# Optimization experiments

Hardware: AMD Instinct MI355X
Metric: run time of the kernel (lower is better)

## Reference

```python
import jax, jax.numpy as jnp
import numpy as np

NUM_NODES = 1_200_000
NUM_FILLER = 200_000
NUM_PHYS = NUM_NODES - NUM_FILLER  # 1,000,000 physical nodes
NUM_MOVABLE = 900_000
NBX = NBY = 512
XL, XH, YL, YH = 0.0, 1000.0, 0.0, 1000.0
BSX = (XH - XL) / NBX
BSY = (YH - YL) / NBY
PIN_STRETCH = 1.4142135623730951
UNIT_PIN_CAP = 0.05
MAX_RATE = 1.5
MIN_RATE = 1.0 / MAX_RATE
K = 5  # max bins overlapped per dimension (span<=4.0, bin~1.95)


def _overlap_terms(lo, hi, bin_size, origin, nb):
    # lo, hi: [n] interval per node. Returns bin indices [n,K] and overlap lengths [n,K].
    il = jnp.clip(jnp.floor((lo - origin) / bin_size).astype(jnp.int32), 0, nb - 1)
    idx = il[:, None] + jnp.arange(K, dtype=jnp.int32)[None, :]
    valid = idx < nb
    idx = jnp.clip(idx, 0, nb - 1)
    b_lo = origin + idx.astype(lo.dtype) * bin_size
    ov = jnp.maximum(jnp.minimum(hi[:, None], b_lo + bin_size) - jnp.maximum(lo[:, None], b_lo), 0.0)
    return idx, jnp.where(valid, ov, 0.0)


def _forward(pos, node_size_x, node_size_y, flat_node2pin_start_map):
    P = NUM_PHYS
    sx, sy = node_size_x[:P], node_size_y[:P]
    # stretched half sizes: at least half a stretched bin
    hx = 0.5 * jnp.maximum(BSX * PIN_STRETCH, sx)
    hy = 0.5 * jnp.maximum(BSY * PIN_STRETCH, sy)
    cx = pos[:P] + 0.5 * sx
    cy = pos[NUM_NODES:NUM_NODES + P] + 0.5 * sy
    pw = (flat_node2pin_start_map[1:P + 1] - flat_node2pin_start_map[:P]).astype(pos.dtype)
    density = pw / (4.0 * hx * hy)  # pins per unit area over stretched bbox

    # stage 1: scatter stretched-bbox pin density into bin map
    ix, ovx = _overlap_terms(cx - hx, cx + hx, BSX, XL, NBX)  # [P,K]
    iy, ovy = _overlap_terms(cy - hy, cy + hy, BSY, YL, NBY)  # [P,K]
    contrib = ovx[:, :, None] * ovy[:, None, :] * density[:, None, None]  # [P,K,K]
    flat_idx = (ix[:, :, None] * NBY + iy[:, None, :]).reshape(-1)
    pin_map = jnp.zeros(NBX * NBY, dtype=pos.dtype).at[flat_idx].add(contrib.reshape(-1))

    # stage 2: pin utilization per bin, clamped adjust rate
    util = jnp.clip(pin_map / (BSX * BSY * UNIT_PIN_CAP), MIN_RATE, MAX_RATE)

    # stage 3: per movable node, integrate utilization over its (unstretched) bbox
    M = NUM_MOVABLE
    x_lo = pos[:M]
    x_hi = x_lo + node_size_x[:M]
    y_lo = pos[NUM_NODES:NUM_NODES + M]
    y_hi = y_lo + node_size_y[:M]
    jx, wx = _overlap_terms(x_lo, x_hi, BSX, XL, NBX)  # [M,K]
    jy, wy = _overlap_terms(y_lo, y_hi, BSY, YL, NBY)  # [M,K]
    u = util[jx[:, :, None] * NBY + jy[:, None, :]]  # [M,K,K]
    instance_pin_area = jnp.sum(wx[:, :, None] * wy[:, None, :] * u, axis=(1, 2))
    return instance_pin_area


def setup_inputs() -> dict:
    key = jax.random.key(0)
    k1, k2, k3, k4 = jax.random.split(key, 4)
    node_size_x = jax.random.uniform(k1, (NUM_NODES,), jnp.float32, 1.0, 4.0)
    node_size_y = jnp.full((NUM_NODES,), 2.0, jnp.float32)  # row height
    px = jax.random.uniform(k2, (NUM_NODES,), jnp.float32, 0.0, 995.0)
    py = jax.random.uniform(k3, (NUM_NODES,), jnp.float32, 0.0, 995.0)
    pos = jnp.concatenate([px, py])
    pin_counts = jax.random.randint(k4, (NUM_PHYS,), 1, 9, jnp.int32)
    flat = jnp.concatenate([jnp.zeros(1, jnp.int32), jnp.cumsum(pin_counts).astype(jnp.int32)])
    return {"pos": pos, "node_size_x": node_size_x, "node_size_y": node_size_y,
            "flat_node2pin_start_map": flat}


def reference(pos, node_size_x, node_size_y, flat_node2pin_start_map):
    return _forward(pos, node_size_x, node_size_y, flat_node2pin_start_map)
```

## Files before the change

kernel.cpp:

```cpp
#include <hip/hip_runtime.h>

#define NUM_NODES   1200000
#define NUM_FILLER  200000
#define NUM_PHYS    (NUM_NODES - NUM_FILLER)
#define NUM_MOVABLE 900000
#define NBX 512
#define NBY 512
#define NBINS (NBX * NBY)
#define BSX 1.953125f
#define BSY 1.953125f
#define PIN_STRETCH 1.4142135623730951f
#define CAP 0.19073486328125f
#define INV_CAP (1.0f / 0.19073486328125f)
#define MAX_RATE 1.5f
#define MIN_RATE (1.0f/1.5f)
#define K 5

#define TBITS   5
#define TSZ     32
#define TDIM    16
#define NTILES  (TDIM * TDIM)
#define HALO    3
#define LTS     (TSZ + HALO)
#define NPB     2048
#define NBLK    ((NUM_PHYS + NPB - 1) / NPB)
#define CAPSLOT 6144

__device__ __forceinline__ int bin_lo(float lo) {
    int il = (int)floorf(lo / BSX);
    return min(max(il, 0), NBX - 1);
}

__global__ __launch_bounds__(256) void sort_pass(
    const float* __restrict__ pos,
    const float* __restrict__ nsx,
    const float* __restrict__ nsy,
    const int*   __restrict__ flat,
    int*         __restrict__ tileCursor,
    float4*      __restrict__ sorted4,
    float*       __restrict__ dens)
{
    __shared__ int cnt[NTILES];
    __shared__ int basep[NTILES];
    int tid = threadIdx.x;
    cnt[tid] = 0;
    __syncthreads();

    float lox[NPB/256], loy[NPB/256], hix[NPB/256], hiy[NPB/256], dn[NPB/256];
    int tl[NPB/256];
    int base = blockIdx.x * NPB;
    #pragma unroll
    for (int it = 0; it < NPB / 256; ++it) {
        int i = base + it * 256 + tid;
        tl[it] = -1;
        if (i < NUM_PHYS) {
            float sx = nsx[i], sy = nsy[i];
            float hx = 0.5f * fmaxf(BSX * PIN_STRETCH, sx);
            float hy = 0.5f * fmaxf(BSY * PIN_STRETCH, sy);
            float cx = pos[i] + 0.5f * sx;
            float cy = pos[NUM_NODES + i] + 0.5f * sy;
            float pw = (float)(flat[i + 1] - flat[i]);
            dn[it]  = pw / (4.0f * hx * hy);
            lox[it] = cx - hx; hix[it] = cx + hx;
            loy[it] = cy - hy; hiy[it] = cy + hy;
            int il = bin_lo(lox[it]), jl = bin_lo(loy[it]);
            tl[it] = ((il >> TBITS) << 4) | (jl >> TBITS);
            atomicAdd(&cnt[tl[it]], 1);
        }
    }
    __syncthreads();
    int c = cnt[tid];
    int b = (c > 0) ? atomicAdd(&tileCursor[tid], c) : 0;
    basep[tid] = b;
    __syncthreads();
    #pragma unroll
    for (int it = 0; it < NPB / 256; ++it) {
        if (tl[it] >= 0) {
            int slot = atomicAdd(&basep[tl[it]], 1);
            if (slot < CAPSLOT) {
                size_t g = (size_t)tl[it] * CAPSLOT + slot;
                sorted4[g] = make_float4(lox[it], loy[it], hix[it], hiy[it]);
                dens[g] = dn[it];
            }
        }
    }
}

__global__ __launch_bounds__(1024) void accumulate_tiles(
    const float4* __restrict__ sorted4,
    const float*  __restrict__ dens,
    const int*    __restrict__ tileCursor,
    float*        __restrict__ pin)
{
    __shared__ float tileA[LTS * LTS];
    int tid = threadIdx.x;
    int t = blockIdx.x;
    int bx0 = (t >> 4) * TSZ, by0 = (t & 15) * TSZ;

    for (int i = tid; i < LTS * LTS; i += 1024) tileA[i] = 0.0f;
    __syncthreads();

    int cnt = min(tileCursor[t], CAPSLOT);
    size_t b0 = (size_t)t * CAPSLOT;
    for (int i = tid; i < cnt; i += 1024) {
        float4 r = sorted4[b0 + i];
        float d = dens[b0 + i];
        int il = bin_lo(r.x), jl = bin_lo(r.y);
        int ie = min(min((int)floorf(r.z / BSX), NBX - 1), il + HALO);
        int je = min(min((int)floorf(r.w / BSY), NBY - 1), jl + HALO);
        int lr = il - bx0, lc = jl - by0;
        for (int a = il; a <= ie; ++a) {
            float blo = (float)a * BSX;
            float ox = fmaxf(fminf(r.z, blo + BSX) - fmaxf(r.x, blo), 0.0f);
            int rowb = (lr + (a - il)) * LTS + lc;
            for (int b2 = jl; b2 <= je; ++b2) {
                float blo2 = (float)b2 * BSY;
                float oy = fmaxf(fminf(r.w, blo2 + BSY) - fmaxf(r.y, blo2), 0.0f);
                float cc = ox * oy * d;
                if (cc != 0.0f) atomicAdd(&tileA[rowb + (b2 - jl)], cc);
            }
        }
    }
    __syncthreads();
    for (int i = tid; i < LTS * LTS; i += 1024) {
        float v = tileA[i];
        if (v != 0.0f) {
            int r = i / LTS, c = i % LTS;
            int gx = bx0 + r, gy = by0 + c;
            if (gx < NBX && gy < NBY) atomicAdd(&pin[gx * NBY + gy], v);
        }
    }
}

__global__ __launch_bounds__(256) void gather_pin_area(
    const float* __restrict__ pos,
    const float* __restrict__ nsx,
    const float* __restrict__ nsy,
    const float* __restrict__ pin,
    float*       __restrict__ out)
{
    int m = blockIdx.x * blockDim.x + threadIdx.x;
    if (m >= NUM_MOVABLE) return;

    float xlo = pos[m];
    float xhi = xlo + nsx[m];
    float ylo = pos[NUM_NODES + m];
    float yhi = ylo + nsy[m];

    int il = bin_lo(xlo);
    int ie = min(min((int)floorf(xhi / BSX), NBX - 1), il + K - 1);
    int jl = bin_lo(ylo);
    int je = min(min((int)floorf(yhi / BSY), NBY - 1), jl + K - 1);

    float acc = 0.0f;
    for (int a = il; a <= ie; ++a) {
        float blo = (float)a * BSX;
        float wxv = fmaxf(fminf(xhi, blo + BSX) - fmaxf(xlo, blo), 0.0f);
        const float* __restrict__ row = pin + a * NBY;
        for (int b2 = jl; b2 <= je; ++b2) {
            float blo2 = (float)b2 * BSY;
            float wyv = fmaxf(fminf(yhi, blo2 + BSY) - fmaxf(ylo, blo2), 0.0f);
            float u = fminf(fmaxf(row[b2] * INV_CAP, MIN_RATE), MAX_RATE);
            acc += wxv * wyv * u;
        }
    }
    out[m] = acc;
}

__global__ __launch_bounds__(256) void scatter_pin_map_agent(
    const float* __restrict__ pos,
    const float* __restrict__ nsx,
    const float* __restrict__ nsy,
    const int*   __restrict__ flat,
    float*       __restrict__ map)
{
    int p = blockIdx.x * blockDim.x + threadIdx.x;
    if (p >= NUM_PHYS) return;
    float sx = nsx[p], sy = nsy[p];
    float hx = 0.5f * fmaxf(BSX * PIN_STRETCH, sx);
    float hy = 0.5f * fmaxf(BSY * PIN_STRETCH, sy);
    float cx = pos[p] + 0.5f * sx;
    float cy = pos[NUM_NODES + p] + 0.5f * sy;
    float pw = (float)(flat[p + 1] - flat[p]);
    float density = pw / (4.0f * hx * hy);
    float lox = cx - hx, hixv = cx + hx;
    float loy = cy - hy, hiyv = cy + hy;
    int il = bin_lo(lox), jl = bin_lo(loy);
    int ie = min(min((int)floorf(hixv / BSX), NBX - 1), il + K - 1);
    int je = min(min((int)floorf(hiyv / BSY), NBY - 1), jl + K - 1);
    for (int a = il; a <= ie; ++a) {
        float blo = (float)a * BSX;
        float ox = fmaxf(fminf(hixv, blo + BSX) - fmaxf(lox, blo), 0.0f);
        for (int b = jl; b <= je; ++b) {
            float blo2 = (float)b * BSY;
            float oy = fmaxf(fminf(hiyv, blo2 + BSY) - fmaxf(loy, blo2), 0.0f);
            float c = ox * oy * density;
            if (c != 0.0f) atomicAdd(&map[a * NBY + b], c);
        }
    }
}

extern "C" void kernel_launch(void* const* d_in, const int* in_sizes, int n_in,
                              void* d_out, int out_size, void* d_ws, size_t ws_size,
                              hipStream_t stream) {
    const float* pos  = (const float*)d_in[0];
    const float* nsx  = (const float*)d_in[1];
    const float* nsy  = (const float*)d_in[2];
    const int*   flat = (const int*)d_in[3];
    float* out = (float*)d_out;

    float* pin = (float*)d_ws;
    int* tileCursor = (int*)((char*)d_ws + (size_t)NBINS * 4);
    float4* sorted4 = (float4*)((char*)d_ws + (size_t)NBINS * 4 + 8192);
    float* dens = (float*)(sorted4 + (size_t)NTILES * CAPSLOT);
    size_t needed = (size_t)NBINS * 4 + 8192
                  + (size_t)NTILES * CAPSLOT * 20;

    dim3 blk(256);
    if (ws_size >= needed) {
        hipMemsetAsync(d_ws, 0, (size_t)NBINS * 4 + 8192, stream);
        sort_pass<<<NBLK, blk, 0, stream>>>(pos, nsx, nsy, flat, tileCursor, sorted4, dens);
        accumulate_tiles<<<NTILES, dim3(1024), 0, stream>>>(sorted4, dens, tileCursor, pin);
    } else {
        hipMemsetAsync(pin, 0, (size_t)NBINS * 4, stream);
        scatter_pin_map_agent<<<(NUM_PHYS + 255) / 256, blk, 0, stream>>>(pos, nsx, nsy, flat, pin);
    }
    gather_pin_area<<<(NUM_MOVABLE + 255) / 256, blk, 0, stream>>>(pos, nsx, nsy, pin, out);
}
```

Measured before the change: 149.5 us.

## Bin-sort movable nodes by tile and gather utilization from shared-memory patches

The sort pass now also buckets movable nodes into 32x32-bin tiles, writing their bboxes and original indices alongside the physical-node records. A new tiled gather kernel loads each tile's clamped utilization patch (with halo) into LDS once, then integrates over it for every node in the tile and scatters each result back to its original index. The aim is to replace random global reads of the pin map with LDS reads. In exchange it adds a second sorted buffer to write and read, scattered output writes, only 256 gather blocks, and per-tile capacity limits that drop nodes if a tile overflows. The halo also grows from 3 to 4.

Result: slower. 156.0 us (+4.3%).

```diff
diff --git a/kernel.cpp b/kernel.cpp
--- a/kernel.cpp
+++ b/kernel.cpp
@@ -20,76 +20,103 @@
 #define TSZ     32
 #define TDIM    16
 #define NTILES  (TDIM * TDIM)
-#define HALO    3
+#define HALO    (K - 1)
 #define LTS     (TSZ + HALO)
 #define NPB     2048
 #define NBLK    ((NUM_PHYS + NPB - 1) / NPB)
-#define CAPSLOT 6144
+#define CAPP    6144
+#define CAPM    5120
 
 __device__ __forceinline__ int bin_lo(float lo) {
     int il = (int)floorf(lo / BSX);
     return min(max(il, 0), NBX - 1);
 }
 
-__global__ __launch_bounds__(256) void sort_pass(
+__global__ __launch_bounds__(256) void sort_both(
     const float* __restrict__ pos,
     const float* __restrict__ nsx,
     const float* __restrict__ nsy,
     const int*   __restrict__ flat,
-    int*         __restrict__ tileCursor,
-    float4*      __restrict__ sorted4,
-    float*       __restrict__ dens)
-{
-    __shared__ int cnt[NTILES];
-    __shared__ int basep[NTILES];
+    int*         __restrict__ physCur,
+    int*         __restrict__ movCur,
+    float4*      __restrict__ physRec,
+    float*       __restrict__ physDens,
+    float4*      __restrict__ movRec,
+    int*         __restrict__ movIdx)
+{
+    __shared__ int cntP[NTILES], cntM[NTILES], baseP[NTILES], baseM[NTILES];
     int tid = threadIdx.x;
-    cnt[tid] = 0;
-    __syncthreads();
-
-    float lox[NPB/256], loy[NPB/256], hix[NPB/256], hiy[NPB/256], dn[NPB/256];
-    int tl[NPB/256];
+    cntP[tid] = 0; cntM[tid] = 0;
+    __syncthreads();
+
+    float px[NPB/256], py[NPB/256], sx[NPB/256], sy[NPB/256], dn[NPB/256];
+    int pk[NPB/256];
     int base = blockIdx.x * NPB;
     #pragma unroll
     for (int it = 0; it < NPB / 256; ++it) {
         int i = base + it * 256 + tid;
-        tl[it] = -1;
+        int k = 0;
         if (i < NUM_PHYS) {
-            float sx = nsx[i], sy = nsy[i];
-            float hx = 0.5f * fmaxf(BSX * PIN_STRETCH, sx);
-            float hy = 0.5f * fmaxf(BSY * PIN_STRETCH, sy);
-            float cx = pos[i] + 0.5f * sx;
-            float cy = pos[NUM_NODES + i] + 0.5f * sy;
+            float pxv = pos[i], pyv = pos[NUM_NODES + i];
+            float sxv = nsx[i], syv = nsy[i];
+            float hx = 0.5f * fmaxf(BSX * PIN_STRETCH, sxv);
+            float hy = 0.5f * fmaxf(BSY * PIN_STRETCH, syv);
             float pw = (float)(flat[i + 1] - flat[i]);
-            dn[it]  = pw / (4.0f * hx * hy);
-            lox[it] = cx - hx; hix[it] = cx + hx;
-            loy[it] = cy - hy; hiy[it] = cy + hy;
-            int il = bin_lo(lox[it]), jl = bin_lo(loy[it]);
-            tl[it] = ((il >> TBITS) << 4) | (jl >> TBITS);
-            atomicAdd(&cnt[tl[it]], 1);
-        }
-    }
-    __syncthreads();
-    int c = cnt[tid];
-    int b = (c > 0) ? atomicAdd(&tileCursor[tid], c) : 0;
-    basep[tid] = b;
-    __syncthreads();
+            px[it] = pxv; py[it] = pyv; sx[it] = sxv; sy[it] = syv;
+            dn[it] = pw / (4.0f * hx * hy);
+            float lox = pxv + 0.5f * sxv - hx;
+            float loy = pyv + 0.5f * syv - hy;
+            int tp = ((bin_lo(lox) >> TBITS) << 4) | (bin_lo(loy) >> TBITS);
+            atomicAdd(&cntP[tp], 1);
+            k = 0x10000 | tp;
+            if (i < NUM_MOVABLE) {
+                int tm = ((bin_lo(pxv) >> TBITS) << 4) | (bin_lo(pyv) >> TBITS);
+                atomicAdd(&cntM[tm], 1);
+                k |= 0x20000 | (tm << 8);
+            }
+        }
+        pk[it] = k;
+    }
+    __syncthreads();
+    int cp = cntP[tid], cm = cntM[tid];
+    baseP[tid] = (cp > 0) ? atomicAdd(&physCur[tid], cp) : 0;
+    baseM[tid] = (cm > 0) ? atomicAdd(&movCur[tid],  cm) : 0;
+    __syncthreads();
+    int i0 = base + tid;
     #pragma unroll
     for (int it = 0; it < NPB / 256; ++it) {
-        if (tl[it] >= 0) {
-            int slot = atomicAdd(&basep[tl[it]], 1);
-            if (slot < CAPSLOT) {
-                size_t g = (size_t)tl[it] * CAPSLOT + slot;
-                sorted4[g] = make_float4(lox[it], loy[it], hix[it], hiy[it]);
-                dens[g] = dn[it];
+        int k = pk[it];
+        if (k & 0x10000) {
+            float sxv = sx[it], syv = sy[it];
+            float hx = 0.5f * fmaxf(BSX * PIN_STRETCH, sxv);
+            float hy = 0.5f * fmaxf(BSY * PIN_STRETCH, syv);
+            float lox = px[it] + 0.5f * sxv - hx;
+            float loy = py[it] + 0.5f * syv - hy;
+            int tp = k & 0xFF;
+            int s = atomicAdd(&baseP[tp], 1);
+            if (s < CAPP) {
+                size_t g = (size_t)tp * CAPP + s;
+                physRec[g] = make_float4(lox, loy, lox + 2.0f * hx, loy + 2.0f * hy);
+                physDens[g] = dn[it];
+            }
+        }
+        if (k & 0x20000) {
+            int tm = (k >> 8) & 0xFF;
+            int s = atomicAdd(&baseM[tm], 1);
+            if (s < CAPM) {
+                size_t g = (size_t)tm * CAPM + s;
+                movRec[g] = make_float4(px[it], py[it],
+                                        px[it] + sx[it], py[it] + sy[it]);
+                movIdx[g] = i0 + it * 256;
             }
         }
     }
 }
 
 __global__ __launch_bounds__(1024) void accumulate_tiles(
-    const float4* __restrict__ sorted4,
-    const float*  __restrict__ dens,
-    const int*    __restrict__ tileCursor,
+    const float4* __restrict__ physRec,
+    const float*  __restrict__ physDens,
+    const int*    __restrict__ physCur,
     float*        __restrict__ pin)
 {
     __shared__ float tileA[LTS * LTS];
@@ -100,11 +127,11 @@
     for (int i = tid; i < LTS * LTS; i += 1024) tileA[i] = 0.0f;
     __syncthreads();
 
-    int cnt = min(tileCursor[t], CAPSLOT);
-    size_t b0 = (size_t)t * CAPSLOT;
+    int cnt = min(physCur[t], CAPP);
+    size_t b0 = (size_t)t * CAPP;
     for (int i = tid; i < cnt; i += 1024) {
-        float4 r = sorted4[b0 + i];
-        float d = dens[b0 + i];
+        float4 r = physRec[b0 + i];
+        float d = physDens[b0 + i];
         int il = bin_lo(r.x), jl = bin_lo(r.y);
         int ie = min(min((int)floorf(r.z / BSX), NBX - 1), il + HALO);
         int je = min(min((int)floorf(r.w / BSY), NBY - 1), jl + HALO);
@@ -132,39 +159,50 @@
     }
 }
 
-__global__ __launch_bounds__(256) void gather_pin_area(
-    const float* __restrict__ pos,
-    const float* __restrict__ nsx,
-    const float* __restrict__ nsy,
-    const float* __restrict__ pin,
-    float*       __restrict__ out)
-{
-    int m = blockIdx.x * blockDim.x + threadIdx.x;
-    if (m >= NUM_MOVABLE) return;
-
-    float xlo = pos[m];
-    float xhi = xlo + nsx[m];
-    float ylo = pos[NUM_NODES + m];
-    float yhi = ylo + nsy[m];
-
-    int il = bin_lo(xlo);
-    int ie = min(min((int)floorf(xhi / BSX), NBX - 1), il + K - 1);
-    int jl = bin_lo(ylo);
-    int je = min(min((int)floorf(yhi / BSY), NBY - 1), jl + K - 1);
-
-    float acc = 0.0f;
-    for (int a = il; a <= ie; ++a) {
-        float blo = (float)a * BSX;
-        float wxv = fmaxf(fminf(xhi, blo + BSX) - fmaxf(xlo, blo), 0.0f);
-        const float* __restrict__ row = pin + a * NBY;
-        for (int b2 = jl; b2 <= je; ++b2) {
-            float blo2 = (float)b2 * BSY;
-            float wyv = fmaxf(fminf(yhi, blo2 + BSY) - fmaxf(ylo, blo2), 0.0f);
-            float u = fminf(fmaxf(row[b2] * INV_CAP, MIN_RATE), MAX_RATE);
-            acc += wxv * wyv * u;
-        }
-    }
-    out[m] = acc;
+__global__ __launch_bounds__(1024) void gather_tiled(
+    const float4* __restrict__ movRec,
+    const int*    __restrict__ movIdx,
+    const int*    __restrict__ movCur,
+    const float*  __restrict__ pin,
+    float*        __restrict__ out)
+{
+    __shared__ float patch[LTS * LTS];
+    int tid = threadIdx.x;
+    int t = blockIdx.x;
+    int bx0 = (t >> 4) * TSZ, by0 = (t & 15) * TSZ;
+
+    for (int i = tid; i < LTS * LTS; i += 1024) {
+        int r = i / LTS, c = i % LTS;
+        int gx = bx0 + r, gy = by0 + c;
+        float u = MIN_RATE;
+        if (gx < NBX && gy < NBY)
+            u = fminf(fmaxf(pin[gx * NBY + gy] * INV_CAP, MIN_RATE), MAX_RATE);
+        patch[i] = u;
+    }
+    __syncthreads();
+
+    int cnt = min(movCur[t], CAPM);
+    size_t b0 = (size_t)t * CAPM;
+    for (int i = tid; i < cnt; i += 1024) {
+        float4 r = movRec[b0 + i];
+        int idx = movIdx[b0 + i];
+        int il = bin_lo(r.x), jl = bin_lo(r.y);
+        int ie = min(min((int)floorf(r.z / BSX), NBX - 1), il + K - 1);
+        int je = min(min((int)floorf(r.w / BSY), NBY - 1), jl + K - 1);
+        int lr = il - bx0, lc = jl - by0;
+        float acc = 0.0f;
+        for (int a = il; a <= ie; ++a) {
+            float blo = (float)a * BSX;
+            float wxv = fmaxf(fminf(r.z, blo + BSX) - fmaxf(r.x, blo), 0.0f);
+            int rowb = (lr + (a - il)) * LTS + lc;
+            for (int b2 = jl; b2 <= je; ++b2) {
+                float blo2 = (float)b2 * BSY;
+                float wyv = fmaxf(fminf(r.w, blo2 + BSY) - fmaxf(r.y, blo2), 0.0f);
+                acc += wxv * wyv * patch[rowb + (b2 - jl)];
+            }
+        }
+        out[idx] = acc;
+    }
 }
 
 __global__ __launch_bounds__(256) void scatter_pin_map_agent(
@@ -200,6 +238,38 @@
     }
 }
 
+__global__ __launch_bounds__(256) void gather_direct(
+    const float* __restrict__ pos,
+    const float* __restrict__ nsx,
+    const float* __restrict__ nsy,
+    const float* __restrict__ pin,
+    float*       __restrict__ out)
+{
+    int m = blockIdx.x * blockDim.x + threadIdx.x;
+    if (m >= NUM_MOVABLE) return;
+    float xlo = pos[m];
+    float xhi = xlo + nsx[m];
+    float ylo = pos[NUM_NODES + m];
+    float yhi = ylo + nsy[m];
+    int il = bin_lo(xlo);
+    int ie = min(min((int)floorf(xhi / BSX), NBX - 1), il + K - 1);
+    int jl = bin_lo(ylo);
+    int je = min(min((int)floorf(yhi / BSY), NBY - 1), jl + K - 1);
+    float acc = 0.0f;
+    for (int a = il; a <= ie; ++a) {
+        float blo = (float)a * BSX;
+        float wxv = fmaxf(fminf(xhi, blo + BSX) - fmaxf(xlo, blo), 0.0f);
+        const float* __restrict__ row = pin + a * NBY;
+        for (int b2 = jl; b2 <= je; ++b2) {
+            float blo2 = (float)b2 * BSY;
+            float wyv = fmaxf(fminf(yhi, blo2 + BSY) - fmaxf(ylo, blo2), 0.0f);
+            float u = fminf(fmaxf(row[b2] * INV_CAP, MIN_RATE), MAX_RATE);
+            acc += wxv * wyv * u;
+        }
+    }
+    out[m] = acc;
+}
+
 extern "C" void kernel_launch(void* const* d_in, const int* in_sizes, int n_in,
                               void* d_out, int out_size, void* d_ws, size_t ws_size,
                               hipStream_t stream) {
@@ -209,21 +279,28 @@
     const int*   flat = (const int*)d_in[3];
     float* out = (float*)d_out;
 
-    float* pin = (float*)d_ws;
-    int* tileCursor = (int*)((char*)d_ws + (size_t)NBINS * 4);
-    float4* sorted4 = (float4*)((char*)d_ws + (size_t)NBINS * 4 + 8192);
-    float* dens = (float*)(sorted4 + (size_t)NTILES * CAPSLOT);
+    char* wsb = (char*)d_ws;
+    float*  pin      = (float*)wsb;
+    int*    physCur  = (int*)(wsb + (size_t)NBINS * 4);
+    int*    movCur   = physCur + NTILES;
+    float4* physRec  = (float4*)(wsb + (size_t)NBINS * 4 + 8192);
+    float*  physDens = (float*)(physRec + (size_t)NTILES * CAPP);
+    float4* movRec   = (float4*)(physDens + (size_t)NTILES * CAPP);
+    int*    movIdx   = (int*)(movRec + (size_t)NTILES * CAPM);
     size_t needed = (size_t)NBINS * 4 + 8192
-                  + (size_t)NTILES * CAPSLOT * 20;
+                  + (size_t)NTILES * CAPP * 20 + (size_t)NTILES * CAPM * 20;
 
     dim3 blk(256);
     if (ws_size >= needed) {
         hipMemsetAsync(d_ws, 0, (size_t)NBINS * 4 + 8192, stream);
-        sort_pass<<<NBLK, blk, 0, stream>>>(pos, nsx, nsy, flat, tileCursor, sorted4, dens);
-        accumulate_tiles<<<NTILES, dim3(1024), 0, stream>>>(sorted4, dens, tileCursor, pin);
+        sort_both<<<NBLK, blk, 0, stream>>>(pos, nsx, nsy, flat,
+                                            physCur, movCur,
+                                            physRec, physDens, movRec, movIdx);
+        accumulate_tiles<<<NTILES, dim3(1024), 0, stream>>>(physRec, physDens, physCur, pin);
+        gather_tiled<<<NTILES, dim3(1024), 0, stream>>>(movRec, movIdx, movCur, pin, out);
     } else {
         hipMemsetAsync(pin, 0, (size_t)NBINS * 4, stream);
         scatter_pin_map_agent<<<(NUM_PHYS + 255) / 256, blk, 0, stream>>>(pos, nsx, nsy, flat, pin);
-    }
-    gather_pin_area<<<(NUM_MOVABLE + 255) / 256, blk, 0, stream>>>(pos, nsx, nsy, pin, out);
-}
+        gather_direct<<<(NUM_MOVABLE + 255) / 256, blk, 0, stream>>>(pos, nsx, nsy, pin, out);
+    }
+}
```

## Partition tile cursors per XCD, enlarge sort blocks, store interior bins directly

Applied to the files above, without the earlier changes.

The bucketing pass now reads the hardware XCC ID and gives each tile a separate cursor and record region per XCD. This is meant to cut cross-die contention on the global atomic cursors. The sort kernel also switches to 1024-thread blocks, each handling 4096 nodes, so fewer blocks issue global cursor atomics. In the accumulate kernel, each tile walks all eight XCD sub-buckets, writes interior bins with plain stores, and keeps atomics only for halo bins. The cost is a larger workspace, a per-tile loop over eight regions, and reliance on an inline-asm hardware register read.

Result: no change. 146.9 us (-1.8%).

```diff
diff --git a/kernel.cpp b/kernel.cpp
--- a/kernel.cpp
+++ b/kernel.cpp
@@ -20,66 +20,75 @@
 #define TSZ     32
 #define TDIM    16
 #define NTILES  (TDIM * TDIM)
-#define HALO    3
+#define HALO    (K - 1)
 #define LTS     (TSZ + HALO)
-#define NPB     2048
+#define NXCD    8
+#define SBLK    1024
+#define NPB     4096
+#define IPT     (NPB / SBLK)
 #define NBLK    ((NUM_PHYS + NPB - 1) / NPB)
-#define CAPSLOT 6144
+#define CAPX    1024
 
 __device__ __forceinline__ int bin_lo(float lo) {
     int il = (int)floorf(lo / BSX);
     return min(max(il, 0), NBX - 1);
 }
 
-__global__ __launch_bounds__(256) void sort_pass(
+__global__ __launch_bounds__(SBLK) void sort_phys(
     const float* __restrict__ pos,
     const float* __restrict__ nsx,
     const float* __restrict__ nsy,
     const int*   __restrict__ flat,
-    int*         __restrict__ tileCursor,
-    float4*      __restrict__ sorted4,
+    int*         __restrict__ cur,
+    float4*      __restrict__ rec,
     float*       __restrict__ dens)
 {
     __shared__ int cnt[NTILES];
     __shared__ int basep[NTILES];
     int tid = threadIdx.x;
-    cnt[tid] = 0;
-    __syncthreads();
-
-    float lox[NPB/256], loy[NPB/256], hix[NPB/256], hiy[NPB/256], dn[NPB/256];
-    int tl[NPB/256];
+    if (tid < NTILES) cnt[tid] = 0;
+    __syncthreads();
+
+    unsigned xcc;
+    asm volatile("s_getreg_b32 %0, hwreg(HW_REG_XCC_ID, 0, 32)" : "=s"(xcc));
+    xcc &= (NXCD - 1);
+
+    float lox[IPT], loy[IPT], hix[IPT], hiy[IPT], dn[IPT];
+    int tl[IPT];
     int base = blockIdx.x * NPB;
     #pragma unroll
-    for (int it = 0; it < NPB / 256; ++it) {
-        int i = base + it * 256 + tid;
+    for (int it = 0; it < IPT; ++it) {
+        int i = base + it * SBLK + tid;
         tl[it] = -1;
         if (i < NUM_PHYS) {
-            float sx = nsx[i], sy = nsy[i];
-            float hx = 0.5f * fmaxf(BSX * PIN_STRETCH, sx);
-            float hy = 0.5f * fmaxf(BSY * PIN_STRETCH, sy);
-            float cx = pos[i] + 0.5f * sx;
-            float cy = pos[NUM_NODES + i] + 0.5f * sy;
+            float sxv = nsx[i], syv = nsy[i];
+            float hx = 0.5f * fmaxf(BSX * PIN_STRETCH, sxv);
+            float hy = 0.5f * fmaxf(BSY * PIN_STRETCH, syv);
+            float cx = pos[i] + 0.5f * sxv;
+            float cy = pos[NUM_NODES + i] + 0.5f * syv;
             float pw = (float)(flat[i + 1] - flat[i]);
             dn[it]  = pw / (4.0f * hx * hy);
             lox[it] = cx - hx; hix[it] = cx + hx;
             loy[it] = cy - hy; hiy[it] = cy + hy;
-            int il = bin_lo(lox[it]), jl = bin_lo(loy[it]);
-            tl[it] = ((il >> TBITS) << 4) | (jl >> TBITS);
-            atomicAdd(&cnt[tl[it]], 1);
-        }
-    }
-    __syncthreads();
-    int c = cnt[tid];
-    int b = (c > 0) ? atomicAdd(&tileCursor[tid], c) : 0;
-    basep[tid] = b;
+            int t = ((bin_lo(lox[it]) >> TBITS) << 4) | (bin_lo(loy[it]) >> TBITS);
+            tl[it] = t;
+            atomicAdd(&cnt[t], 1);
+        }
+    }
+    __syncthreads();
+    if (tid < NTILES) {
+        int c = cnt[tid];
+        basep[tid] = (c > 0) ? atomicAdd(&cur[tid * NXCD + xcc], c) : 0;
+    }
     __syncthreads();
     #pragma unroll
-    for (int it = 0; it < NPB / 256; ++it) {
-        if (tl[it] >= 0) {
-            int slot = atomicAdd(&basep[tl[it]], 1);
-            if (slot < CAPSLOT) {
-                size_t g = (size_t)tl[it] * CAPSLOT + slot;
-                sorted4[g] = make_float4(lox[it], loy[it], hix[it], hiy[it]);
+    for (int it = 0; it < IPT; ++it) {
+        int t = tl[it];
+        if (t >= 0) {
+            int s = atomicAdd(&basep[t], 1);
+            if (s < CAPX) {
+                size_t g = ((size_t)t * NXCD + xcc) * CAPX + s;
+                rec[g] = make_float4(lox[it], loy[it], hix[it], hiy[it]);
                 dens[g] = dn[it];
             }
         }
@@ -87,9 +96,9 @@
 }
 
 __global__ __launch_bounds__(1024) void accumulate_tiles(
-    const float4* __restrict__ sorted4,
+    const float4* __restrict__ rec,
     const float*  __restrict__ dens,
-    const int*    __restrict__ tileCursor,
+    const int*    __restrict__ cur,
     float*        __restrict__ pin)
 {
     __shared__ float tileA[LTS * LTS];
@@ -100,34 +109,40 @@
     for (int i = tid; i < LTS * LTS; i += 1024) tileA[i] = 0.0f;
     __syncthreads();
 
-    int cnt = min(tileCursor[t], CAPSLOT);
-    size_t b0 = (size_t)t * CAPSLOT;
-    for (int i = tid; i < cnt; i += 1024) {
-        float4 r = sorted4[b0 + i];
-        float d = dens[b0 + i];
-        int il = bin_lo(r.x), jl = bin_lo(r.y);
-        int ie = min(min((int)floorf(r.z / BSX), NBX - 1), il + HALO);
-        int je = min(min((int)floorf(r.w / BSY), NBY - 1), jl + HALO);
-        int lr = il - bx0, lc = jl - by0;
-        for (int a = il; a <= ie; ++a) {
-            float blo = (float)a * BSX;
-            float ox = fmaxf(fminf(r.z, blo + BSX) - fmaxf(r.x, blo), 0.0f);
-            int rowb = (lr + (a - il)) * LTS + lc;
-            for (int b2 = jl; b2 <= je; ++b2) {
-                float blo2 = (float)b2 * BSY;
-                float oy = fmaxf(fminf(r.w, blo2 + BSY) - fmaxf(r.y, blo2), 0.0f);
-                float cc = ox * oy * d;
-                if (cc != 0.0f) atomicAdd(&tileA[rowb + (b2 - jl)], cc);
+    for (int x = 0; x < NXCD; ++x) {
+        int cnt = min(cur[t * NXCD + x], CAPX);
+        size_t b0 = ((size_t)t * NXCD + x) * CAPX;
+        for (int i = tid; i < cnt; i += 1024) {
+            float4 r = rec[b0 + i];
+            float d = dens[b0 + i];
+            int il = bin_lo(r.x), jl = bin_lo(r.y);
+            int ie = min(min((int)floorf(r.z / BSX), NBX - 1), il + HALO);
+            int je = min(min((int)floorf(r.w / BSY), NBY - 1), jl + HALO);
+            int lr = il - bx0, lc = jl - by0;
+            for (int a = il; a <= ie; ++a) {
+                float blo = (float)a * BSX;
+                float ox = fmaxf(fminf(r.z, blo + BSX) - fmaxf(r.x, blo), 0.0f);
+                int rowb = (lr + (a - il)) * LTS + lc;
+                for (int b2 = jl; b2 <= je; ++b2) {
+                    float blo2 = (float)b2 * BSY;
+                    float oy = fmaxf(fminf(r.w, blo2 + BSY) - fmaxf(r.y, blo2), 0.0f);
+                    float cc = ox * oy * d;
+                    if (cc != 0.0f) atomicAdd(&tileA[rowb + (b2 - jl)], cc);
+                }
             }
         }
     }
     __syncthreads();
     for (int i = tid; i < LTS * LTS; i += 1024) {
         float v = tileA[i];
-        if (v != 0.0f) {
-            int r = i / LTS, c = i % LTS;
-            int gx = bx0 + r, gy = by0 + c;
-            if (gx < NBX && gy < NBY) atomicAdd(&pin[gx * NBY + gy], v);
+        int r = i / LTS, c = i % LTS;
+        int gx = bx0 + r, gy = by0 + c;
+        if (gx >= NBX || gy >= NBY) continue;
+        bool interior = (r >= HALO) && (r < TSZ) && (c >= HALO) && (c < TSZ);
+        if (interior) {
+            if (v != 0.0f) pin[gx * NBY + gy] = v;
+        } else {
+            if (v != 0.0f) atomicAdd(&pin[gx * NBY + gy], v);
         }
     }
 }
@@ -209,18 +224,19 @@
     const int*   flat = (const int*)d_in[3];
     float* out = (float*)d_out;
 
-    float* pin = (float*)d_ws;
-    int* tileCursor = (int*)((char*)d_ws + (size_t)NBINS * 4);
-    float4* sorted4 = (float4*)((char*)d_ws + (size_t)NBINS * 4 + 8192);
-    float* dens = (float*)(sorted4 + (size_t)NTILES * CAPSLOT);
+    char* wsb = (char*)d_ws;
+    float*  pin  = (float*)wsb;
+    int*    cur  = (int*)(wsb + (size_t)NBINS * 4);
+    float4* rec  = (float4*)(wsb + (size_t)NBINS * 4 + 8192);
+    float*  dens = (float*)(rec + (size_t)NTILES * NXCD * CAPX);
     size_t needed = (size_t)NBINS * 4 + 8192
-                  + (size_t)NTILES * CAPSLOT * 20;
+                  + (size_t)NTILES * NXCD * CAPX * 20;
 
     dim3 blk(256);
     if (ws_size >= needed) {
         hipMemsetAsync(d_ws, 0, (size_t)NBINS * 4 + 8192, stream);
-        sort_pass<<<NBLK, blk, 0, stream>>>(pos, nsx, nsy, flat, tileCursor, sorted4, dens);
-        accumulate_tiles<<<NTILES, dim3(1024), 0, stream>>>(sorted4, dens, tileCursor, pin);
+        sort_phys<<<NBLK, dim3(SBLK), 0, stream>>>(pos, nsx, nsy, flat, cur, rec, dens);
+        accumulate_tiles<<<NTILES, dim3(1024), 0, stream>>>(rec, dens, cur, pin);
     } else {
         hipMemsetAsync(pin, 0, (size_t)NBINS * 4, stream);
         scatter_pin_map_agent<<<(NUM_PHYS + 255) / 256, blk, 0, stream>>>(pos, nsx, nsy, flat, pin);
```
